# Optimization experiments

Measured on AMD Instinct MI355X. Metric: run time of the kernel, lower is better.

The kernel has to match this reference:

```python
import jax, jax.numpy as jnp
import numpy as np

EPS = 1e-5

def _proj_bn(x, w, b, gamma, beta, mean, var):
    # 1x1 conv: [B,C,H,W] x [O,C] -> [B,O,H,W], then inference BatchNorm
    y = jnp.einsum('bchw,oc->bohw', x, w) + b[None, :, None, None]
    inv = gamma / jnp.sqrt(var + EPS)
    return y * inv[None, :, None, None] + (beta - mean * inv)[None, :, None, None]


def setup_inputs() -> dict:
    key = jax.random.key(0)
    ks = jax.random.split(key, 20)
    B, C, H, W = 4, 256, 64, 64
    Cq = C // 8
    s = lambda k, shp, sc: jax.random.normal(k, shp, dtype=jnp.float32) * sc
    inp = {
        'x1': s(ks[0], (B, C, H, W), 1.0),
        'x2': s(ks[1], (B, C, H, W), 1.0),
        'q_w': s(ks[2], (Cq, C), 0.05), 'q_b': s(ks[3], (Cq,), 0.02),
        'q_gamma': 1.0 + s(ks[4], (Cq,), 0.02), 'q_beta': s(ks[5], (Cq,), 0.02),
        'q_mean': s(ks[6], (Cq,), 0.1), 'q_var': jnp.abs(1.0 + s(ks[7], (Cq,), 0.1)),
        'k_w': s(ks[8], (Cq, C), 0.05), 'k_b': s(ks[9], (Cq,), 0.02),
        'k_gamma': 1.0 + s(ks[10], (Cq,), 0.02), 'k_beta': s(ks[11], (Cq,), 0.02),
        'k_mean': s(ks[12], (Cq,), 0.1), 'k_var': jnp.abs(1.0 + s(ks[13], (Cq,), 0.1)),
        'v_w': s(ks[14], (C, C), 0.05), 'v_b': s(ks[15], (C,), 0.02),
        'v_gamma': 1.0 + s(ks[16], (C,), 0.02), 'v_beta': s(ks[17], (C,), 0.02),
        'v_mean': s(ks[18], (C,), 0.1), 'v_var': jnp.abs(1.0 + s(ks[19], (C,), 0.1)),
    }
    return inp


def reference(x1, x2, q_w, q_b, q_gamma, q_beta, q_mean, q_var,
              k_w, k_b, k_gamma, k_beta, k_mean, k_var,
              v_w, v_b, v_gamma, v_beta, v_mean, v_var):
    B, C, H, W = x1.shape
    N = H * W
    dqk = C // 8
    q = _proj_bn(x1, q_w, q_b, q_gamma, q_beta, q_mean, q_var).reshape(B, dqk, N)  # [B,dqk,N]
    k = _proj_bn(x2, k_w, k_b, k_gamma, k_beta, k_mean, k_var).reshape(B, dqk, N)  # [B,dqk,N]
    v = _proj_bn(x2, v_w, v_b, v_gamma, v_beta, v_mean, v_var).reshape(B, C, N)    # [B,C,N]
    scale = 1.0 / np.sqrt(dqk).astype(np.float32)
    energy = jnp.einsum('bdm,bdn->bmn', q, k) * scale        # [B,N,N]
    attn = jax.nn.softmax(energy, axis=-1)
    out = jnp.einsum('bcn,bmn->bcm', v, attn)                # [B,C,N]
    return out.reshape(B, C, H, W)
```

## Files before the change

### kernel.cpp

```cpp
#include <hip/hip_runtime.h>

using short8   = __attribute__((ext_vector_type(8))) short;
using f32x4    = __attribute__((ext_vector_type(4))) float;
using ushort4v = __attribute__((ext_vector_type(4))) unsigned short;

#define BN_EPS 1e-5f
#define ATT_SCALE_LOG2E 0.2550348347988049f

__device__ __forceinline__ unsigned short f2bf(float f) {
    union { float f; unsigned u; } v; v.f = f;
    return (unsigned short)((v.u + 0x7FFFu + ((v.u >> 16) & 1u)) >> 16);
}

__device__ __forceinline__ unsigned pack2bf(float a, float b) {
    union { float f; unsigned u; } ua, ub; ua.f = a; ub.f = b;
    return __builtin_amdgcn_perm(ub.u + 0x8000u, ua.u + 0x8000u, 0x07060302u);
}

__device__ __forceinline__ void glds16(const void* gp, void* lp) {
    __builtin_amdgcn_global_load_lds(
        (const __attribute__((address_space(1))) unsigned*)gp,
        (__attribute__((address_space(3))) unsigned*)lp, 16, 0, 0);
}

__global__ void prep_kernel(
    const float* __restrict__ qw, const float* __restrict__ qb,
    const float* __restrict__ qg, const float* __restrict__ qbe,
    const float* __restrict__ qm, const float* __restrict__ qv,
    const float* __restrict__ kw, const float* __restrict__ kb,
    const float* __restrict__ kg, const float* __restrict__ kbe,
    const float* __restrict__ km, const float* __restrict__ kvv,
    const float* __restrict__ vw, const float* __restrict__ vb,
    const float* __restrict__ vg, const float* __restrict__ vbe,
    const float* __restrict__ vm, const float* __restrict__ vv,
    unsigned short* __restrict__ wq, float* __restrict__ scale,
    float* __restrict__ off)
{
    int r = blockIdx.x;
    int t = threadIdx.x;
    const float *wsrc, *g, *be, *mn, *vr, *bi;
    int rl;
    if (r < 32)      { rl = r;      wsrc = qw; g = qg; be = qbe; mn = qm; vr = qv;  bi = qb; }
    else if (r < 64) { rl = r - 32; wsrc = kw; g = kg; be = kbe; mn = km; vr = kvv; bi = kb; }
    else             { rl = r - 64; wsrc = vw; g = vg; be = vbe; mn = vm; vr = vv;  bi = vb; }

    float4 w4 = *(const float4*)(wsrc + rl * 256 + t * 4);
    ushort4v o;
    o.x = f2bf(w4.x); o.y = f2bf(w4.y); o.z = f2bf(w4.z); o.w = f2bf(w4.w);
    *(ushort4v*)(wq + r * 256 + t * 4) = o;

    if (t == 0) {
        float inv = g[rl] * rsqrtf(vr[rl] + BN_EPS);
        float ofv = bi[rl] * inv + be[rl] - mn[rl] * inv;
        float s = (r < 32) ? ATT_SCALE_LOG2E : 1.0f;
        scale[r] = inv * s;
        off[r]   = ofv * s;
    }
}

#define XT_PITCH 264

__global__ __launch_bounds__(256, 4) void proj_kernel(
    const float* __restrict__ x1, const float* __restrict__ x2,
    const unsigned short* __restrict__ wq,
    const float* __restrict__ scale, const float* __restrict__ off,
    unsigned short* __restrict__ q_t, unsigned short* __restrict__ k_t,
    unsigned short* __restrict__ v_ws)
{
    __shared__ __align__(16) unsigned short Xt[64 * XT_PITCH];
    int bx = blockIdx.x;
    int g  = bx >> 8;
    int t2 = bx & 255;
    int nt = t2 & 63;
    int b  = t2 >> 6;
    int n0 = nt * 64;
    int tid = threadIdx.x;
    int wv = tid >> 6, lane = tid & 63;
    int m16 = lane & 15, qd = lane >> 4;

    const float* xb = ((g == 0) ? x1 : x2) + (size_t)b * 256 * 4096 + n0 + lane;

    #pragma unroll 2
    for (int i = 0; i < 8; ++i) {
        int o = wv * 8 + i;
        const float* src = xb + (size_t)(o * 8) * 4096;
        uint4 dw;
        dw.x = pack2bf(src[0],                src[(size_t)1 * 4096]);
        dw.y = pack2bf(src[(size_t)2 * 4096], src[(size_t)3 * 4096]);
        dw.z = pack2bf(src[(size_t)4 * 4096], src[(size_t)5 * 4096]);
        dw.w = pack2bf(src[(size_t)6 * 4096], src[(size_t)7 * 4096]);
        *(uint4*)&Xt[lane * XT_PITCH + o * 8] = dw;
    }
    __syncthreads();

    f32x4 zero4 = {0.f, 0.f, 0.f, 0.f};

    if (g < 2) {
        int rb = g * 32;
        f32x4 acc0 = zero4, acc1 = zero4;
        #pragma unroll 2
        for (int s = 0; s < 8; ++s) {
            short8 w0 = *(const short8*)(wq + (size_t)(rb +      m16) * 256 + s * 32 + qd * 8);
            short8 w1 = *(const short8*)(wq + (size_t)(rb + 16 + m16) * 256 + s * 32 + qd * 8);
            short8 xf = *(const short8*)&Xt[(16 * wv + m16) * XT_PITCH + s * 32 + qd * 8];
            acc0 = __builtin_amdgcn_mfma_f32_16x16x32_bf16(w0, xf, acc0, 0, 0, 0);
            acc1 = __builtin_amdgcn_mfma_f32_16x16x32_bf16(w1, xf, acc1, 0, 0, 0);
        }
        unsigned short* dst = (g == 0) ? q_t : k_t;
        int ncol = n0 + 16 * wv + m16;
        #pragma unroll
        for (int tm = 0; tm < 2; ++tm) {
            f32x4 acc = tm ? acc1 : acc0;
            int r0 = 16 * tm + 4 * qd;
            float4 sc = *(const float4*)(scale + rb + r0);
            float4 of = *(const float4*)(off   + rb + r0);
            ushort4v o;
            o.x = f2bf(acc.x * sc.x + of.x);
            o.y = f2bf(acc.y * sc.y + of.y);
            o.z = f2bf(acc.z * sc.z + of.z);
            o.w = f2bf(acc.w * sc.w + of.w);
            *(ushort4v*)(dst + ((size_t)b * 4096 + ncol) * 32 + r0) = o;
        }
    } else {
        f32x4 acc[4][4];
        #pragma unroll
        for (int rr = 0; rr < 4; ++rr)
            #pragma unroll
            for (int tm = 0; tm < 4; ++tm) acc[rr][tm] = zero4;
        #pragma unroll 1
        for (int s = 0; s < 8; ++s) {
            short8 xf[4];
            #pragma unroll
            for (int tm = 0; tm < 4; ++tm)
                xf[tm] = *(const short8*)&Xt[(16 * tm + m16) * XT_PITCH + s * 32 + qd * 8];
            #pragma unroll
            for (int rr = 0; rr < 4; ++rr) {
                short8 wf = *(const short8*)(wq + (size_t)(64 + rr * 64 + 16 * wv + m16) * 256 + s * 32 + qd * 8);
                #pragma unroll
                for (int tm = 0; tm < 4; ++tm)
                    acc[rr][tm] = __builtin_amdgcn_mfma_f32_16x16x32_bf16(xf[tm], wf, acc[rr][tm], 0, 0, 0);
            }
        }
        unsigned short* vt = v_ws + (size_t)(b * 64 + nt) * 256 * 64;
        #pragma unroll
        for (int rr = 0; rr < 4; ++rr) {
            int c = rr * 64 + 16 * wv + m16;
            float sc = scale[64 + c], of = off[64 + c];
            #pragma unroll
            for (int tm = 0; tm < 4; ++tm) {
                int nloc = 16 * tm + 4 * qd;
                ushort4v o;
                o.x = f2bf(acc[rr][tm].x * sc + of);
                o.y = f2bf(acc[rr][tm].y * sc + of);
                o.z = f2bf(acc[rr][tm].z * sc + of);
                o.w = f2bf(acc[rr][tm].w * sc + of);
                *(ushort4v*)(vt + c * 64 + nloc) = o;
            }
        }
    }
}

__global__ __launch_bounds__(256, 2) void flash_kernel(
    const unsigned short* __restrict__ q_t, const unsigned short* __restrict__ k_t,
    const unsigned short* __restrict__ v_ws, float* __restrict__ out)
{
    __shared__ __align__(16) unsigned char Smem[50176];

    int bx = blockIdx.x;
    int cg = (bx >> 2) & 1;
    int b  = bx & 3;
    int qg = bx >> 3;
    int q0 = qg * 64;
    int cb = cg * 128;

    int tid = threadIdx.x;
    int wv  = tid >> 6, lane = tid & 63;
    int m16 = lane & 15, qd = lane >> 4;
    int sw7 = m16 & 7, sw3 = m16 & 3;

    char* smem = (char*)Smem;
    unsigned short* Ps = (unsigned short*)(smem + 40960);
    float*          Lsh = (float*)(smem + 49152);

    int kgo, kl = wv * 1024;
    { int i = wv * 64 + lane; int row = i >> 2, pos = i & 3;
      kgo = (row * 4 + (pos ^ (row & 3))) * 16; }
    int vgo[4], vl[4];
    #pragma unroll
    for (int u = 0; u < 4; ++u) {
        int i = (wv * 4 + u) * 64 + lane; int row = i >> 3, pos = i & 7;
        vgo[u] = (row * 8 + (pos ^ (row & 7))) * 16;
        vl[u]  = (wv * 4 + u) * 1024;
    }

    const char* kbase = (const char*)k_t + (size_t)b * 262144;
    const char* vbase = (const char*)v_ws + (size_t)b * 2097152 + (size_t)cb * 128;

    const unsigned short* qb = q_t + ((size_t)b * 4096 + q0) * 32;
    short8 Qf[4];
    #pragma unroll
    for (int qt = 0; qt < 4; ++qt)
        Qf[qt] = *(const short8*)(qb + (size_t)(qt * 16 + m16) * 32 + qd * 8);

    int kro = (wv * 16 + m16) * 64 + ((qd ^ sw3) << 4);
    int widx[4];
    #pragma unroll
    for (int qt = 0; qt < 4; ++qt)
        widx[qt] = (qt * 16 + m16) * 64 + (((wv * 2 + (qd >> 1)) ^ sw7) << 3) + ((qd & 1) << 2);
    int vro[2];
    #pragma unroll
    for (int kc = 0; kc < 2; ++kc)
        vro[kc] = ((kc * 4 + qd) ^ sw7) << 4;

    f32x4 zero4 = {0.f, 0.f, 0.f, 0.f};
    f32x4 acc[4][2];
    #pragma unroll
    for (int qt = 0; qt < 4; ++qt)
        #pragma unroll
        for (int ct = 0; ct < 2; ++ct) acc[qt][ct] = zero4;
    float lsum[4] = {0.f, 0.f, 0.f, 0.f};

    glds16(kbase + kgo, smem + kl);
    #pragma unroll
    for (int u = 0; u < 4; ++u) glds16(vbase + vgo[u], smem + 8192 + vl[u]);

    #pragma unroll 1
    for (int it = 0; it < 64; ++it) {
        int z = it & 1;
        char* Kb = smem + z * 4096;
        char* Vb = smem + 8192 + z * 16384;

        asm volatile("s_waitcnt vmcnt(0)\n\ts_barrier" ::: "memory");

        short8 Kf = *(const short8*)(Kb + kro);

        if (it < 63) {
            const char* ks = kbase + (size_t)(it + 1) * 4096;
            const char* vs = vbase + (size_t)(it + 1) * 32768;
            char* kd = smem + (z ^ 1) * 4096;
            char* vd = smem + 8192 + (z ^ 1) * 16384;
            glds16(ks + kgo, kd + kl);
            #pragma unroll
            for (int u = 0; u < 4; ++u) glds16(vs + vgo[u], vd + vl[u]);
        }

        short8 Vf[2][2];
        #pragma unroll
        for (int ct = 0; ct < 2; ++ct)
            #pragma unroll
            for (int kc = 0; kc < 2; ++kc)
                Vf[ct][kc] = *(const short8*)(Vb + (wv * 32 + ct * 16 + m16) * 128 + vro[kc]);

        #pragma unroll
        for (int qt = 0; qt < 4; ++qt) {
            f32x4 S = __builtin_amdgcn_mfma_f32_16x16x32_bf16(Kf, Qf[qt], zero4, 0, 0, 0);
            float a0 = __builtin_amdgcn_exp2f(S.x), a1 = __builtin_amdgcn_exp2f(S.y);
            float a2 = __builtin_amdgcn_exp2f(S.z), a3 = __builtin_amdgcn_exp2f(S.w);
            lsum[qt] += (a0 + a1) + (a2 + a3);
            uint2 w; w.x = pack2bf(a0, a1); w.y = pack2bf(a2, a3);
            *(uint2*)&Ps[widx[qt]] = w;
        }

        asm volatile("s_waitcnt lgkmcnt(0)\n\ts_barrier" ::: "memory");

        __builtin_amdgcn_s_setprio(1);
        short8 Ap[4][2];
        #pragma unroll
        for (int qt = 0; qt < 4; ++qt)
            #pragma unroll
            for (int kc = 0; kc < 2; ++kc)
                Ap[qt][kc] = *(const short8*)&Ps[(qt * 16 + m16) * 64 + (((kc * 4 + qd) ^ sw7) << 3)];
        #pragma unroll
        for (int qt = 0; qt < 4; ++qt)
            #pragma unroll
            for (int ct = 0; ct < 2; ++ct) {
                acc[qt][ct] = __builtin_amdgcn_mfma_f32_16x16x32_bf16(Ap[qt][0], Vf[ct][0], acc[qt][ct], 0, 0, 0);
                acc[qt][ct] = __builtin_amdgcn_mfma_f32_16x16x32_bf16(Ap[qt][1], Vf[ct][1], acc[qt][ct], 0, 0, 0);
            }
        __builtin_amdgcn_s_setprio(0);
    }

    #pragma unroll
    for (int qt = 0; qt < 4; ++qt) {
        float l = lsum[qt];
        l += __shfl_xor(l, 16);
        l += __shfl_xor(l, 32);
        if (lane < 16) Lsh[wv * 64 + qt * 16 + lane] = l;
    }
    asm volatile("s_waitcnt lgkmcnt(0)\n\ts_barrier" ::: "memory");

    #pragma unroll
    for (int qt = 0; qt < 4; ++qt) {
        f32x4 s4 = *(const f32x4*)&Lsh[qt * 16 + qd * 4];
        s4 += *(const f32x4*)&Lsh[64  + qt * 16 + qd * 4];
        s4 += *(const f32x4*)&Lsh[128 + qt * 16 + qd * 4];
        s4 += *(const f32x4*)&Lsh[192 + qt * 16 + qd * 4];
        f32x4 inv4;
        inv4.x = __builtin_amdgcn_rcpf(s4.x);
        inv4.y = __builtin_amdgcn_rcpf(s4.y);
        inv4.z = __builtin_amdgcn_rcpf(s4.z);
        inv4.w = __builtin_amdgcn_rcpf(s4.w);
        #pragma unroll
        for (int ct = 0; ct < 2; ++ct) {
            float* ob = out + ((size_t)(b * 256 + cb + wv * 32 + ct * 16 + m16)) * 4096
                            + q0 + qt * 16 + qd * 4;
            float4 o;
            o.x = acc[qt][ct].x * inv4.x;
            o.y = acc[qt][ct].y * inv4.y;
            o.z = acc[qt][ct].z * inv4.z;
            o.w = acc[qt][ct].w * inv4.w;
            *(float4*)ob = o;
        }
    }
}

extern "C" void kernel_launch(void* const* d_in, const int* in_sizes, int n_in,
                              void* d_out, int out_size, void* d_ws, size_t ws_size,
                              hipStream_t stream)
{
    const float* x1  = (const float*)d_in[0];
    const float* x2  = (const float*)d_in[1];
    const float* qw  = (const float*)d_in[2];
    const float* qb  = (const float*)d_in[3];
    const float* qg  = (const float*)d_in[4];
    const float* qbe = (const float*)d_in[5];
    const float* qm  = (const float*)d_in[6];
    const float* qv  = (const float*)d_in[7];
    const float* kw  = (const float*)d_in[8];
    const float* kb  = (const float*)d_in[9];
    const float* kg  = (const float*)d_in[10];
    const float* kbe = (const float*)d_in[11];
    const float* km  = (const float*)d_in[12];
    const float* kvv = (const float*)d_in[13];
    const float* vw  = (const float*)d_in[14];
    const float* vb  = (const float*)d_in[15];
    const float* vg  = (const float*)d_in[16];
    const float* vbe = (const float*)d_in[17];
    const float* vm  = (const float*)d_in[18];
    const float* vv  = (const float*)d_in[19];

    char* ws = (char*)d_ws;
    unsigned short* wq   = (unsigned short*)(ws + 0);
    float*          scale= (float*)(ws + 163840);
    float*          off  = (float*)(ws + 165120);
    unsigned short* q_t  = (unsigned short*)(ws + 166400);
    unsigned short* k_t  = (unsigned short*)(ws + 166400 + 1048576);
    unsigned short* v_ws = (unsigned short*)(ws + 166400 + 2097152);

    prep_kernel<<<320, 64, 0, stream>>>(qw, qb, qg, qbe, qm, qv,
                                        kw, kb, kg, kbe, km, kvv,
                                        vw, vb, vg, vbe, vm, vv,
                                        wq, scale, off);
    proj_kernel<<<768, 256, 0, stream>>>(x1, x2, wq, scale, off, q_t, k_t, v_ws);
    flash_kernel<<<512, 256, 0, stream>>>(q_t, k_t, v_ws, (float*)d_out);
}
```

Baseline: 185.2 us.

## Load K/V fragments directly into registers with register double-buffering instead of LDS staging

```diff
diff --git a/kernel.cpp b/kernel.cpp
--- a/kernel.cpp
+++ b/kernel.cpp
@@ -15,12 +15,6 @@
 __device__ __forceinline__ unsigned pack2bf(float a, float b) {
     union { float f; unsigned u; } ua, ub; ua.f = a; ub.f = b;
     return __builtin_amdgcn_perm(ub.u + 0x8000u, ua.u + 0x8000u, 0x07060302u);
-}
-
-__device__ __forceinline__ void glds16(const void* gp, void* lp) {
-    __builtin_amdgcn_global_load_lds(
-        (const __attribute__((address_space(1))) unsigned*)gp,
-        (__attribute__((address_space(3))) unsigned*)lp, 16, 0, 0);
 }
 
 __global__ void prep_kernel(
@@ -164,7 +158,8 @@
     const unsigned short* __restrict__ q_t, const unsigned short* __restrict__ k_t,
     const unsigned short* __restrict__ v_ws, float* __restrict__ out)
 {
-    __shared__ __align__(16) unsigned char Smem[50176];
+    __shared__ __align__(16) unsigned short Ps[64 * 64];
+    __shared__ __align__(16) float Lsh[256];
 
     int bx = blockIdx.x;
     int cg = (bx >> 2) & 1;
@@ -176,25 +171,11 @@
     int tid = threadIdx.x;
     int wv  = tid >> 6, lane = tid & 63;
     int m16 = lane & 15, qd = lane >> 4;
-    int sw7 = m16 & 7, sw3 = m16 & 3;
-
-    char* smem = (char*)Smem;
-    unsigned short* Ps = (unsigned short*)(smem + 40960);
-    float*          Lsh = (float*)(smem + 49152);
-
-    int kgo, kl = wv * 1024;
-    { int i = wv * 64 + lane; int row = i >> 2, pos = i & 3;
-      kgo = (row * 4 + (pos ^ (row & 3))) * 16; }
-    int vgo[4], vl[4];
-    #pragma unroll
-    for (int u = 0; u < 4; ++u) {
-        int i = (wv * 4 + u) * 64 + lane; int row = i >> 3, pos = i & 7;
-        vgo[u] = (row * 8 + (pos ^ (row & 7))) * 16;
-        vl[u]  = (wv * 4 + u) * 1024;
-    }
-
-    const char* kbase = (const char*)k_t + (size_t)b * 262144;
-    const char* vbase = (const char*)v_ws + (size_t)b * 2097152 + (size_t)cb * 128;
+    int sw7 = m16 & 7;
+
+    const unsigned short* kbase = k_t + ((size_t)b * 4096 + wv * 16 + m16) * 32 + qd * 8;
+    const unsigned short* vbase = v_ws + (size_t)b * 1048576
+                                + (size_t)(cb + wv * 32 + m16) * 64 + qd * 8;
 
     const unsigned short* qb = q_t + ((size_t)b * 4096 + q0) * 32;
     short8 Qf[4];
@@ -202,15 +183,16 @@
     for (int qt = 0; qt < 4; ++qt)
         Qf[qt] = *(const short8*)(qb + (size_t)(qt * 16 + m16) * 32 + qd * 8);
 
-    int kro = (wv * 16 + m16) * 64 + ((qd ^ sw3) << 4);
     int widx[4];
     #pragma unroll
     for (int qt = 0; qt < 4; ++qt)
         widx[qt] = (qt * 16 + m16) * 64 + (((wv * 2 + (qd >> 1)) ^ sw7) << 3) + ((qd & 1) << 2);
-    int vro[2];
-    #pragma unroll
-    for (int kc = 0; kc < 2; ++kc)
-        vro[kc] = ((kc * 4 + qd) ^ sw7) << 4;
+    int apo[4][2];
+    #pragma unroll
+    for (int qt = 0; qt < 4; ++qt)
+        #pragma unroll
+        for (int kc = 0; kc < 2; ++kc)
+            apo[qt][kc] = (qt * 16 + m16) * 64 + (((kc * 4 + qd) ^ sw7) << 3);
 
     f32x4 zero4 = {0.f, 0.f, 0.f, 0.f};
     f32x4 acc[4][2];
@@ -220,40 +202,28 @@
         for (int ct = 0; ct < 2; ++ct) acc[qt][ct] = zero4;
     float lsum[4] = {0.f, 0.f, 0.f, 0.f};
 
-    glds16(kbase + kgo, smem + kl);
-    #pragma unroll
-    for (int u = 0; u < 4; ++u) glds16(vbase + vgo[u], smem + 8192 + vl[u]);
-
-    #pragma unroll 1
-    for (int it = 0; it < 64; ++it) {
-        int z = it & 1;
-        char* Kb = smem + z * 4096;
-        char* Vb = smem + 8192 + z * 16384;
-
-        asm volatile("s_waitcnt vmcnt(0)\n\ts_barrier" ::: "memory");
-
-        short8 Kf = *(const short8*)(Kb + kro);
-
-        if (it < 63) {
-            const char* ks = kbase + (size_t)(it + 1) * 4096;
-            const char* vs = vbase + (size_t)(it + 1) * 32768;
-            char* kd = smem + (z ^ 1) * 4096;
-            char* vd = smem + 8192 + (z ^ 1) * 16384;
-            glds16(ks + kgo, kd + kl);
-            #pragma unroll
-            for (int u = 0; u < 4; ++u) glds16(vs + vgo[u], vd + vl[u]);
-        }
-
-        short8 Vf[2][2];
+    short8 KA, KB, VA[2][2], VB[2][2];
+    KA = *(const short8*)kbase;
+    #pragma unroll
+    for (int ct = 0; ct < 2; ++ct)
+        #pragma unroll
+        for (int kc = 0; kc < 2; ++kc)
+            VA[ct][kc] = *(const short8*)(vbase + ct * 1024 + kc * 32);
+
+    auto body = [&](short8& Kc, short8 (&Vc)[2][2],
+                    short8& Kn, short8 (&Vn)[2][2], int nx) {
+        asm volatile("s_barrier" ::: "memory");
+
+        Kn = *(const short8*)(kbase + (size_t)nx * 2048);
         #pragma unroll
         for (int ct = 0; ct < 2; ++ct)
             #pragma unroll
             for (int kc = 0; kc < 2; ++kc)
-                Vf[ct][kc] = *(const short8*)(Vb + (wv * 32 + ct * 16 + m16) * 128 + vro[kc]);
+                Vn[ct][kc] = *(const short8*)(vbase + (size_t)nx * 16384 + ct * 1024 + kc * 32);
 
         #pragma unroll
         for (int qt = 0; qt < 4; ++qt) {
-            f32x4 S = __builtin_amdgcn_mfma_f32_16x16x32_bf16(Kf, Qf[qt], zero4, 0, 0, 0);
+            f32x4 S = __builtin_amdgcn_mfma_f32_16x16x32_bf16(Kc, Qf[qt], zero4, 0, 0, 0);
             float a0 = __builtin_amdgcn_exp2f(S.x), a1 = __builtin_amdgcn_exp2f(S.y);
             float a2 = __builtin_amdgcn_exp2f(S.z), a3 = __builtin_amdgcn_exp2f(S.w);
             lsum[qt] += (a0 + a1) + (a2 + a3);
@@ -269,15 +239,21 @@
         for (int qt = 0; qt < 4; ++qt)
             #pragma unroll
             for (int kc = 0; kc < 2; ++kc)
-                Ap[qt][kc] = *(const short8*)&Ps[(qt * 16 + m16) * 64 + (((kc * 4 + qd) ^ sw7) << 3)];
+                Ap[qt][kc] = *(const short8*)&Ps[apo[qt][kc]];
         #pragma unroll
         for (int qt = 0; qt < 4; ++qt)
             #pragma unroll
             for (int ct = 0; ct < 2; ++ct) {
-                acc[qt][ct] = __builtin_amdgcn_mfma_f32_16x16x32_bf16(Ap[qt][0], Vf[ct][0], acc[qt][ct], 0, 0, 0);
-                acc[qt][ct] = __builtin_amdgcn_mfma_f32_16x16x32_bf16(Ap[qt][1], Vf[ct][1], acc[qt][ct], 0, 0, 0);
+                acc[qt][ct] = __builtin_amdgcn_mfma_f32_16x16x32_bf16(Ap[qt][0], Vc[ct][0], acc[qt][ct], 0, 0, 0);
+                acc[qt][ct] = __builtin_amdgcn_mfma_f32_16x16x32_bf16(Ap[qt][1], Vc[ct][1], acc[qt][ct], 0, 0, 0);
             }
         __builtin_amdgcn_s_setprio(0);
+    };
+
+    #pragma unroll 1
+    for (int it = 0; it < 64; it += 2) {
+        body(KA, VA, KB, VB, it + 1);
+        body(KB, VB, KA, VA, (it + 2 > 63) ? 63 : it + 2);
     }
 
     #pragma unroll
```

After: 192.2 us. 3.8% more time.
